# Kernel optimization log

Measured on AMD Instinct MI355X. Metric: run time of the kernel, lower is better.

The kernel has to match this reference:

```python
import jax, jax.numpy as jnp
import numpy as np

LN_EPS = 1e-5
WKV_EPS = 1e-8


def _layernorm(x, g, b):
    mu = jnp.mean(x, axis=-1, keepdims=True)
    var = jnp.mean((x - mu) ** 2, axis=-1, keepdims=True)
    return (x - mu) * jax.lax.rsqrt(var + LN_EPS) * g + b


def setup_inputs() -> dict:
    key = jax.random.key(0)
    ks = jax.random.split(key, 16)
    B, S, D, F = 4, 2048, 1024, 4096
    xavier_d = float(np.sqrt(6.0 / (D + D)))
    xavier_df = float(np.sqrt(6.0 / (D + F)))
    u = lambda k, sh, s: jax.random.uniform(k, sh, jnp.float32, -s, s)
    return {
        "x": jax.random.normal(ks[0], (B, S, D), jnp.float32),
        "ln1_g": jnp.ones((D,), jnp.float32),
        "ln1_b": jnp.zeros((D,), jnp.float32),
        "ln2_g": jnp.ones((D,), jnp.float32),
        "ln2_b": jnp.zeros((D,), jnp.float32),
        "Wr": u(ks[1], (D, D), xavier_d),
        "Ww": u(ks[2], (D, D), xavier_d),
        "Wk": u(ks[3], (D, D), xavier_d),
        "Wv": u(ks[4], (D, D), xavier_d),
        "Wo": u(ks[5], (D, D), xavier_d),
        "time_decay": jax.random.uniform(ks[6], (D,), jnp.float32, -1.0, 0.0),
        "time_first": jax.random.uniform(ks[7], (D,), jnp.float32, -1.0, 1.0),
        "Wkey": u(ks[8], (F, D), xavier_df),
        "Wval": u(ks[9], (D, F), xavier_df),
        "Wrec": u(ks[10], (D, D), xavier_d),
    }


def _time_mix(xn, Wr, Ww, Wk, Wv, Wo, time_decay):
    # xn: [B,S,D]
    r = jax.nn.sigmoid(jnp.einsum('bsd,ed->bse', xn, Wr))
    w = -jnp.exp(jnp.einsum('bsd,ed->bse', xn, Ww))
    k = jnp.einsum('bsd,ed->bse', xn, Wk)
    v = jnp.einsum('bsd,ed->bse', xn, Wv)
    ewk = jnp.exp(w + k)  # [B,S,D]
    decay = jnp.exp(time_decay)  # [D]

    def step(carry, inp):
        num, den = carry
        e, vt = inp
        num = decay * num + e * vt
        den = decay * den + e
        wkv = num / (den + WKV_EPS)
        return (num, den), wkv

    B, S, D = xn.shape
    init = (jnp.zeros((B, D), xn.dtype), jnp.zeros((B, D), xn.dtype))
    (num_f, den_f), wkv = jax.lax.scan(
        step, init, (jnp.swapaxes(ewk, 0, 1), jnp.swapaxes(v, 0, 1)))
    wkv = jnp.swapaxes(wkv, 0, 1)  # [B,S,D]
    out = jnp.einsum('bsd,ed->bse', r * wkv, Wo)
    final_state = jnp.stack([num_f, den_f], axis=1)  # [B,2,D]
    return out, final_state


def _channel_mix(xn, Wkey, Wval, Wrec):
    k = jnp.einsum('bsd,fd->bsf', xn, Wkey)
    k = jnp.square(jax.nn.relu(k))
    v = jnp.einsum('bsf,df->bsd', k, Wval)
    r = jax.nn.sigmoid(jnp.einsum('bsd,ed->bse', xn, Wrec))
    return r * v


def reference(x, ln1_g, ln1_b, ln2_g, ln2_b, Wr, Ww, Wk, Wv, Wo,
              time_decay, time_first, Wkey, Wval, Wrec):
    tm, new_state = _time_mix(_layernorm(x, ln1_g, ln1_b),
                              Wr, Ww, Wk, Wv, Wo, time_decay)
    x = x + tm
    x = x + _channel_mix(_layernorm(x, ln2_g, ln2_b), Wkey, Wval, Wrec)
    return x, new_state
```

## Files before the change

### kernel.cpp

```cpp
#include <hip/hip_runtime.h>
#include <hip/hip_bf16.h>
#include <cstdint>
#include <cstddef>

using bf16 = __hip_bfloat16;
typedef __bf16 bf16x8 __attribute__((ext_vector_type(8)));
typedef float floatx4 __attribute__((ext_vector_type(4)));

#define LN_EPS 1e-5f
#define WKV_EPS 1e-8f

static constexpr int Bdim = 4, S = 2048, D = 1024, F = 4096;
static constexpr int M = Bdim * S;
static constexpr int NCH = 64, CH = S / NCH;
static constexpr uint32_t FP32_MAGIC = 0x3F800000u;

__device__ __forceinline__ bool is_fp32(const uint32_t* flagp) {
    return *flagp == FP32_MAGIC;
}
__device__ __forceinline__ float loadf(const void* p, size_t i, bool f32) {
    return f32 ? ((const float*)p)[i] : __bfloat162float(((const bf16*)p)[i]);
}

__device__ __forceinline__ void gload_lds16(const void* g, void* l) {
    __builtin_amdgcn_global_load_lds(
        (__attribute__((address_space(1))) void*)(g),
        (__attribute__((address_space(3))) void*)(l), 16, 0, 0);
}

__device__ __forceinline__ bf16x8 sigmoid8(bf16x8 v) {
    bf16x8 o;
    #pragma unroll
    for (int e = 0; e < 8; e++) {
        const float f = (float)v[e];
        o[e] = (__bf16)(1.0f / (1.0f + __expf(-f)));
    }
    return o;
}
__device__ __forceinline__ bf16x8 relusq8(bf16x8 v) {
    bf16x8 o;
    #pragma unroll
    for (int e = 0; e < 8; e++) {
        const float f = fmaxf((float)v[e], 0.0f);
        o[e] = (__bf16)(f * f);
    }
    return o;
}

struct WcvtArgs {
    const void* src[7];
    bf16*       dst[7];
};
__global__ __launch_bounds__(256)
void wcvt(WcvtArgs a, const uint32_t* __restrict__ flagp)
{
    const bool f32 = is_fp32(flagp);
    const int64_t idx = (int64_t)blockIdx.x * 256 + threadIdx.x;
    int seg, off;
    if (idx < (int64_t)6 * 1048576) {
        seg = (int)(idx >> 20); off = (int)(idx & 1048575);
    } else {
        seg = 6; off = (int)(idx - (int64_t)6 * 1048576);
    }
    a.dst[seg][off] = __float2bfloat16(loadf(a.src[seg], off, f32));
}
__global__ __launch_bounds__(256)
void wcvt2(const void* __restrict__ src, bf16* __restrict__ dst,
           const uint32_t* __restrict__ flagp)
{
    const bool f32 = is_fp32(flagp);
    const int idx = blockIdx.x * 256 + threadIdx.x;
    dst[idx] = __float2bfloat16(loadf(src, idx, f32));
}

enum { EPI_QKVW = 1, EPI_KR = 2, EPI_ADDX = 3, EPI_FINAL = 4 };

struct QkvwOut { bf16 *r, *g, *k, *v; };

template<int EPI>
__global__ __launch_bounds__(512, 4)
void gemm_bt(const bf16* __restrict__ A, const bf16* __restrict__ Bw,
             void* __restrict__ outp, const void* __restrict__ aux1,
             void* __restrict__ aux2, QkvwOut qo, int K, int N,
             const uint32_t* __restrict__ flagp)
{
    __shared__ __align__(16) bf16 smem[16384];
    char* smb = (char*)smem;
    const int t = threadIdx.x;
    const int tn = blockIdx.x, tm = blockIdx.y;
    const int lane = t & 63, wv = t >> 6;
    const int wm = wv & 1, wn = wv >> 1;
    const int ml = lane & 15, quad = lane >> 4;

    const size_t rowB = (size_t)K * 2;
    const int r0 = t >> 3;
    const int q0 = (t & 7) ^ (r0 & 7);
    const char* gA = (const char*)(A)  + (size_t)(tm * 128) * rowB;
    const char* gB = (const char*)(Bw) + (size_t)(tn * 128) * rowB;
    const char* a0 = gA + (size_t)r0 * rowB + q0 * 16;
    const char* a1 = a0 + 64 * rowB;
    const char* b0 = gB + (size_t)r0 * rowB + q0 * 16;
    const char* b1 = b0 + 64 * rowB;
    char* lA0 = smb + t * 16;
    char* lA1 = smb + t * 16 + 8192;
    char* lB0 = smb + t * 16 + 16384;
    char* lB1 = smb + t * 16 + 24576;

    floatx4 acc[4][2] = {};
    const int m7 = ml & 7;
    const int rq0 = ((quad)     ^ m7) * 16;
    const int rq1 = ((4 + quad) ^ m7) * 16;

    for (int k0 = 0; k0 < K; k0 += 64) {
        gload_lds16(a0, lA0);
        gload_lds16(a1, lA1);
        gload_lds16(b0, lB0);
        gload_lds16(b1, lB1);
        a0 += 128; a1 += 128; b0 += 128; b1 += 128;
        __syncthreads();
        #pragma unroll
        for (int kh = 0; kh < 2; kh++) {
            const int rq = kh ? rq1 : rq0;
            bf16x8 af[4], bfr[2];
            #pragma unroll
            for (int i = 0; i < 4; i++)
                af[i]  = *(const bf16x8*)(smb + (wm * 64 + i * 16 + ml) * 128 + rq);
            #pragma unroll
            for (int j = 0; j < 2; j++)
                bfr[j] = *(const bf16x8*)(smb + 16384 + (wn * 32 + j * 16 + ml) * 128 + rq);
            #pragma unroll
            for (int i = 0; i < 4; i++)
                #pragma unroll
                for (int j = 0; j < 2; j++)
                    acc[i][j] = __builtin_amdgcn_mfma_f32_16x16x32_bf16(af[i], bfr[j], acc[i][j], 0, 0, 0);
        }
        __syncthreads();
    }

    const bool f32 = is_fp32(flagp);
    constexpr int PS = 136;
    const int lwr = wm * 16 + quad * 4;
    const int lwc = wn * 32 + ml;
    const int rr = t >> 4;
    const int rc = (t & 15) * 8;
    #pragma unroll
    for (int i = 0; i < 4; i++) {
        __syncthreads();
        #pragma unroll
        for (int j = 0; j < 2; j++)
            #pragma unroll
            for (int rg = 0; rg < 4; rg++)
                smem[(lwr + rg) * PS + lwc + j * 16] = __float2bfloat16(acc[i][j][rg]);
        __syncthreads();
        const int gr = tm * 128 + ((rr < 16) ? (i * 16 + rr) : (64 + i * 16 + rr - 16));
        bf16x8 v = *(const bf16x8*)&smem[rr * PS + rc];
        const int gcol = tn * 128 + rc;
        if constexpr (EPI == EPI_QKVW) {
            const int seg = tn >> 3;
            bf16* dst = (seg == 0) ? qo.r : (seg == 1) ? qo.g : (seg == 2) ? qo.k : qo.v;
            const size_t i2 = (size_t)gr * 1024 + (gcol & 1023);
            if (seg == 0) v = sigmoid8(v);
            *(bf16x8*)&dst[i2] = v;
        } else if constexpr (EPI == EPI_KR) {
            if (tn < 8) {
                *(bf16x8*)&((bf16*)aux2)[(size_t)gr * 1024 + gcol] = sigmoid8(v);
            } else {
                *(bf16x8*)&((bf16*)outp)[(size_t)gr * 4096 + (gcol - 1024)] = relusq8(v);
            }
        } else if constexpr (EPI == EPI_ADDX) {
            const size_t idx = (size_t)gr * N + gcol;
            bf16x8 o;
            if (f32) {
                const float4* xp = (const float4*)((const float*)aux1 + idx);
                const float4 xa = xp[0], xb = xp[1];
                o[0] = (__bf16)((float)v[0] + xa.x); o[1] = (__bf16)((float)v[1] + xa.y);
                o[2] = (__bf16)((float)v[2] + xa.z); o[3] = (__bf16)((float)v[3] + xa.w);
                o[4] = (__bf16)((float)v[4] + xb.x); o[5] = (__bf16)((float)v[5] + xb.y);
                o[6] = (__bf16)((float)v[6] + xb.z); o[7] = (__bf16)((float)v[7] + xb.w);
            } else {
                const bf16x8 xv = *(const bf16x8*)((const bf16*)aux1 + idx);
                #pragma unroll
                for (int e = 0; e < 8; e++) o[e] = (__bf16)((float)v[e] + (float)xv[e]);
            }
            *(bf16x8*)((bf16*)outp + idx) = o;
        } else {
            const size_t idx = (size_t)gr * N + gcol;
            const bf16x8 x2v = *(const bf16x8*)((const bf16*)aux1 + idx);
            const bf16x8 rv  = *(const bf16x8*)((const bf16*)aux2 + idx);
            float ov[8];
            #pragma unroll
            for (int e = 0; e < 8; e++)
                ov[e] = (float)x2v[e] + (float)rv[e] * (float)v[e];
            if (f32) {
                float4 f0 = { ov[0], ov[1], ov[2], ov[3] };
                float4 f1 = { ov[4], ov[5], ov[6], ov[7] };
                float4* op = (float4*)((float*)outp + idx);
                op[0] = f0; op[1] = f1;
            } else {
                bf16x8 o;
                #pragma unroll
                for (int e = 0; e < 8; e++) o[e] = (__bf16)ov[e];
                *(bf16x8*)((bf16*)outp + idx) = o;
            }
        }
    }
}

#define BARR  __builtin_amdgcn_s_barrier()
#define LGKM0 asm volatile("s_waitcnt lgkmcnt(0)" ::: "memory")
#define CFENCE asm volatile("" ::: "memory")

#define LDA256(d, mh) do { \
    _Pragma("unroll") for (int il = 0; il < 4; il++) \
    _Pragma("unroll") for (int kh = 0; kh < 2; kh++) \
        af[il][kh] = *(const bf16x8*)(smem + (d) * 65536 + \
            (wm * 128 + ((mh) * 4 + il) * 16 + ml) * 128 + rq[kh]); \
} while (0)

#define LDB256(d, nh) do { \
    _Pragma("unroll") for (int jl = 0; jl < 2; jl++) \
    _Pragma("unroll") for (int kh = 0; kh < 2; kh++) \
        bfr[jl][kh] = *(const bf16x8*)(smem + (d) * 65536 + 32768 + \
            (wn * 64 + ((nh) * 2 + jl) * 16 + ml) * 128 + rq[kh]); \
} while (0)

#define MMA256(mh, nh) do { \
    _Pragma("unroll") for (int il = 0; il < 4; il++) \
    _Pragma("unroll") for (int jl = 0; jl < 2; jl++) \
    _Pragma("unroll") for (int kh = 0; kh < 2; kh++) \
        acc[(mh) * 4 + il][(nh) * 2 + jl] = __builtin_amdgcn_mfma_f32_16x16x32_bf16( \
            af[il][kh], bfr[jl][kh], acc[(mh) * 4 + il][(nh) * 2 + jl], 0, 0, 0); \
} while (0)

#define STAGE_A256(d, h, kb) do { \
    gload_lds16(gA + (size_t)(h) * 128 * rowB + (kb), smem + (d) * 65536 + (h) * 16384 + t * 16); \
    gload_lds16(gA + ((size_t)(h) * 128 + 64) * rowB + (kb), smem + (d) * 65536 + (h) * 16384 + 8192 + t * 16); \
} while (0)

#define STAGE_B256(d, h, kb) do { \
    gload_lds16(gB + (size_t)(h) * 128 * rowB + (kb), smem + (d) * 65536 + 32768 + (h) * 16384 + t * 16); \
    gload_lds16(gB + ((size_t)(h) * 128 + 64) * rowB + (kb), smem + (d) * 65536 + 32768 + (h) * 16384 + 8192 + t * 16); \
} while (0)

#define PH_MID() do { BARR; LGKM0; __builtin_amdgcn_s_setprio(1); } while (0)
#define PH_END() do { __builtin_amdgcn_s_setprio(0); BARR; } while (0)

template<int EPI>
__global__ __launch_bounds__(512)
void gemm256(const bf16* __restrict__ A, const bf16* __restrict__ Bw,
             void* __restrict__ outp, const void* __restrict__ aux1,
             void* __restrict__ aux2, QkvwOut qo, int K, int N,
             const uint32_t* __restrict__ flagp)
{
    __shared__ __align__(16) char smem[131072];
    (void)N; (void)aux1; (void)flagp;
    const int t = threadIdx.x;
    const int tn = blockIdx.x, tm = blockIdx.y;
    const int lane = t & 63, wv = t >> 6;
    const int wm = wv & 1, wn = wv >> 1;
    const int ml = lane & 15, quad = lane >> 4;

    const size_t rowB = (size_t)K * 2;
    const int r0 = t >> 3;
    const int q0 = (t & 7) ^ (r0 & 7);
    const char* gA = (const char*)(A)  + (size_t)(tm * 256) * rowB + (size_t)r0 * rowB + q0 * 16;
    const char* gB = (const char*)(Bw) + (size_t)(tn * 256) * rowB + (size_t)r0 * rowB + q0 * 16;

    floatx4 acc[8][4] = {};
    bf16x8 af[4][2], bfr[2][2];
    const int m7 = ml & 7;
    const int rq[2] = { ((quad) ^ m7) * 16, ((4 + quad) ^ m7) * 16 };

    const int NT = K >> 6;
    STAGE_A256(0, 0, (size_t)0);
    STAGE_A256(0, 1, (size_t)0);
    STAGE_B256(0, 0, (size_t)0);
    STAGE_B256(0, 1, (size_t)0);
    const size_t kbp = (size_t)((NT > 1) ? 1 : 0) * 128;
    STAGE_A256(1, 0, kbp);
    STAGE_A256(1, 1, kbp);
    asm volatile("s_waitcnt vmcnt(4)" ::: "memory");
    BARR;

    for (int tt = 0; tt < NT; ++tt) {
        const int d = tt & 1;
        const size_t kb1 = (size_t)((tt + 1 < NT) ? tt + 1 : NT - 1) * 128;
        const size_t kb2 = (size_t)((tt + 2 < NT) ? tt + 2 : NT - 1) * 128;
        LDA256(d, 0); LDB256(d, 0);
        STAGE_B256(d ^ 1, 0, kb1);
        STAGE_B256(d ^ 1, 1, kb1);
        PH_MID(); MMA256(0, 0); PH_END();
        LDB256(d, 1);
        PH_MID(); MMA256(0, 1); PH_END();
        LDA256(d, 1);
        PH_MID(); MMA256(1, 1); PH_END();
        LDB256(d, 0);
        CFENCE;
        STAGE_A256(d, 0, kb2);
        STAGE_A256(d, 1, kb2);
        PH_MID(); MMA256(1, 0);
        asm volatile("s_waitcnt vmcnt(4)" ::: "memory");
        PH_END();
    }
    asm volatile("s_waitcnt vmcnt(0)" ::: "memory");
    BARR;

    bf16* sm = (bf16*)smem;
    constexpr int PS = 264;
    const int rr = t >> 4;
    const int rc = (t & 15) * 16;
    #pragma unroll
    for (int p = 0; p < 8; ++p) {
        __syncthreads();
        if (wm == (p >> 2)) {
            const int i0 = (p & 3) * 2;
            #pragma unroll
            for (int f = 0; f < 2; ++f)
                #pragma unroll
                for (int j = 0; j < 4; ++j)
                    #pragma unroll
                    for (int rg = 0; rg < 4; ++rg)
                        sm[(f * 16 + quad * 4 + rg) * PS + wn * 64 + j * 16 + ml] =
                            __float2bfloat16(acc[i0 + f][j][rg]);
        }
        __syncthreads();
        const int gr = tm * 256 + p * 32 + rr;
        bf16x8 v0 = *(const bf16x8*)&sm[rr * PS + rc];
        bf16x8 v1 = *(const bf16x8*)&sm[rr * PS + rc + 8];
        if constexpr (EPI == EPI_QKVW) {
            const int seg = tn >> 2;
            bf16* dst = (seg == 0) ? qo.r : (seg == 1) ? qo.g : (seg == 2) ? qo.k : qo.v;
            const size_t idx = (size_t)gr * 1024 + (tn & 3) * 256 + rc;
            if (seg == 0) { v0 = sigmoid8(v0); v1 = sigmoid8(v1); }
            *(bf16x8*)&dst[idx] = v0;
            *(bf16x8*)&dst[idx + 8] = v1;
        } else {
            if (tn < 4) {
                bf16* dst = (bf16*)aux2;
                const size_t idx = (size_t)gr * 1024 + tn * 256 + rc;
                *(bf16x8*)&dst[idx] = sigmoid8(v0);
                *(bf16x8*)&dst[idx + 8] = sigmoid8(v1);
            } else {
                bf16* dst = (bf16*)outp;
                const size_t idx = (size_t)gr * 4096 + (tn - 4) * 256 + rc;
                *(bf16x8*)&dst[idx] = relusq8(v0);
                *(bf16x8*)&dst[idx + 8] = relusq8(v1);
            }
        }
    }
}

#undef BARR
#undef LGKM0
#undef CFENCE
#undef LDA256
#undef LDB256
#undef MMA256
#undef STAGE_A256
#undef STAGE_B256
#undef PH_MID
#undef PH_END

template<bool IN_WS>
__global__ __launch_bounds__(256)
void ln_kernel(const void* __restrict__ x, const void* __restrict__ g,
               const void* __restrict__ b, bf16* __restrict__ out,
               const uint32_t* __restrict__ flagp)
{
    const bool f32 = is_fp32(flagp);
    const int row = blockIdx.x;
    const int t = threadIdx.x;
    const size_t base = (size_t)row * D;
    float v[4];
    #pragma unroll
    for (int i = 0; i < 4; i++) {
        const size_t c = base + t + 256 * i;
        if constexpr (IN_WS) v[i] = __bfloat162float(((const bf16*)x)[c]);
        else                 v[i] = loadf(x, c, f32);
    }
    float s = v[0] + v[1] + v[2] + v[3];
    float q = v[0]*v[0] + v[1]*v[1] + v[2]*v[2] + v[3]*v[3];
    #pragma unroll
    for (int off = 32; off > 0; off >>= 1) {
        s += __shfl_down(s, off);
        q += __shfl_down(q, off);
    }
    __shared__ float rs_[4], rq_[4];
    const int wv = t >> 6, lane = t & 63;
    if (lane == 0) { rs_[wv] = s; rq_[wv] = q; }
    __syncthreads();
    const float St = rs_[0] + rs_[1] + rs_[2] + rs_[3];
    const float Qt = rq_[0] + rq_[1] + rq_[2] + rq_[3];
    const float mean = St * (1.0f / 1024.0f);
    const float var  = Qt * (1.0f / 1024.0f) - mean * mean;
    const float rstd = rsqrtf(var + LN_EPS);
    #pragma unroll
    for (int i = 0; i < 4; i++) {
        const int c = t + 256 * i;
        const float gv = loadf(g, c, f32);
        const float bv = loadf(b, c, f32);
        out[base + c] = __float2bfloat16((v[i] - mean) * rstd * gv + bv);
    }
}

__global__ __launch_bounds__(256)
void scan_a(const bf16* __restrict__ gw, const bf16* __restrict__ kk,
            const bf16* __restrict__ vbuf, const void* __restrict__ td,
            float* __restrict__ numc, float* __restrict__ denc,
            const uint32_t* __restrict__ flagp)
{
    const bool f32 = is_fp32(flagp);
    const int idx = blockIdx.x * 256 + threadIdx.x;
    const int d = idx & (D - 1);
    const int c = (idx >> 10) & (NCH - 1);
    const int b = idx >> 16;
    const float a = __expf(loadf(td, d, f32));
    size_t p = ((size_t)b * S + (size_t)c * CH) * D + d;
    float num = 0.f, den = 0.f;
    for (int ts = 0; ts < CH; ts++) {
        const float g  = __bfloat162float(gw[p]);
        const float kv = __bfloat162float(kk[p]);
        const float e  = __expf(kv - __expf(g));
        const float vv = __bfloat162float(vbuf[p]);
        num = fmaf(a, num, e * vv);
        den = fmaf(a, den, e);
        p += D;
    }
    const size_t slot = ((size_t)b * NCH + c) * D + d;
    numc[slot] = num;
    denc[slot] = den;
}

__global__ __launch_bounds__(256)
void scan_b(float* __restrict__ numc, float* __restrict__ denc,
            const void* __restrict__ td, void* __restrict__ d_out,
            const uint32_t* __restrict__ flagp)
{
    const bool f32 = is_fp32(flagp);
    const int idx = blockIdx.x * 256 + threadIdx.x;
    const int d = idx & (D - 1);
    const int b = idx >> 10;
    const float aL = __expf(loadf(td, d, f32) * (float)CH);
    float cn = 0.f, cd = 0.f;
    for (int c = 0; c < NCH; c++) {
        const size_t slot = ((size_t)b * NCH + c) * D + d;
        const float ln = numc[slot], ld = denc[slot];
        numc[slot] = cn;
        denc[slot] = cd;
        cn = fmaf(aL, cn, ln);
        cd = fmaf(aL, cd, ld);
    }
    const size_t i0 = (size_t)b * 2 * D + d;
    const size_t i1 = i0 + D;
    const size_t off = (size_t)M * D;
    if (f32) {
        ((float*)d_out)[off + i0] = cn;
        ((float*)d_out)[off + i1] = cd;
    } else {
        ((bf16*)d_out)[off + i0] = __float2bfloat16(cn);
        ((bf16*)d_out)[off + i1] = __float2bfloat16(cd);
    }
}

__global__ __launch_bounds__(256)
void scan_c(const bf16* __restrict__ gw, const bf16* __restrict__ kk,
            const bf16* __restrict__ vbuf, bf16* __restrict__ rbuf,
            const float* __restrict__ numc, const float* __restrict__ denc,
            const void* __restrict__ td, const uint32_t* __restrict__ flagp)
{
    const bool f32 = is_fp32(flagp);
    const int idx = blockIdx.x * 256 + threadIdx.x;
    const int d = idx & (D - 1);
    const int c = (idx >> 10) & (NCH - 1);
    const int b = idx >> 16;
    const float a = __expf(loadf(td, d, f32));
    const size_t slot = ((size_t)b * NCH + c) * D + d;
    float num = numc[slot], den = denc[slot];
    size_t p = ((size_t)b * S + (size_t)c * CH) * D + d;
    for (int ts = 0; ts < CH; ts++) {
        const float g  = __bfloat162float(gw[p]);
        const float kv = __bfloat162float(kk[p]);
        const float e  = __expf(kv - __expf(g));
        const float vv = __bfloat162float(vbuf[p]);
        num = fmaf(a, num, e * vv);
        den = fmaf(a, den, e);
        const float wkv = num / (den + WKV_EPS);
        const float r = __bfloat162float(rbuf[p]);
        rbuf[p] = __float2bfloat16(r * wkv);
        p += D;
    }
}

extern "C" void kernel_launch(void* const* d_in, const int* in_sizes, int n_in,
                              void* d_out, int out_size, void* d_ws, size_t ws_size,
                              hipStream_t stream)
{
    const void* x     = d_in[0];
    const void* ln1_g = d_in[1];
    const void* ln1_b = d_in[2];
    const void* ln2_g = d_in[3];
    const void* ln2_b = d_in[4];
    const void* Wr    = d_in[5];
    const void* Ww    = d_in[6];
    const void* Wk    = d_in[7];
    const void* Wv    = d_in[8];
    const void* Wo    = d_in[9];
    const void* td    = d_in[10];
    const void* Wkey  = d_in[12];
    const void* Wval  = d_in[13];
    const void* Wrec  = d_in[14];
    const uint32_t* flagp = (const uint32_t*)ln1_g;

    #define MB(x) ((size_t)(x) << 20)
    char* ws = (char*)d_ws;
    bf16*  xnb    = (bf16*) (ws + MB(0));
    bf16*  wWval2 = (bf16*) (ws + MB(0));
    bf16*  gw     = (bf16*) (ws + MB(16));
    bf16*  kk     = (bf16*) (ws + MB(32));
    bf16*  vbuf   = (bf16*) (ws + MB(48));
    bf16*  wqkvw  = (bf16*) (ws + MB(64));
    bf16*  wWo    = (bf16*) (ws + MB(72));
    float* numc   = (float*)(ws + MB(74));
    float* denc   = (float*)(ws + MB(75));
    bf16*  kbuf   = (bf16*) (ws + MB(16));
    bf16*  rbuf   = (bf16*) (ws + MB(80));
    bf16*  x2     = (bf16*) (ws + MB(96));
    bf16*  wrk    = (bf16*) (ws + MB(112));
    #undef MB

    dim3 blk(256);
    dim3 blkG(512);
    dim3 gQ(4096 / 256, M / 256);
    dim3 gKR(5120 / 256, M / 256);
    dim3 gN1(D / 128, M / 128);

    WcvtArgs wa;
    wa.src[0] = Wr;   wa.dst[0] = wqkvw;
    wa.src[1] = Ww;   wa.dst[1] = wqkvw + (size_t)1 * 1048576;
    wa.src[2] = Wk;   wa.dst[2] = wqkvw + (size_t)2 * 1048576;
    wa.src[3] = Wv;   wa.dst[3] = wqkvw + (size_t)3 * 1048576;
    wa.src[4] = Wo;   wa.dst[4] = wWo;
    wa.src[5] = Wrec; wa.dst[5] = wrk;
    wa.src[6] = Wkey; wa.dst[6] = wrk + (size_t)1048576;

    QkvwOut qo = { rbuf, gw, kk, vbuf };
    QkvwOut q0 = { nullptr, nullptr, nullptr, nullptr };

    wcvt<<<(10 * 1048576) / 256, blk, 0, stream>>>(wa, flagp);
    ln_kernel<false><<<M, blk, 0, stream>>>(x, ln1_g, ln1_b, xnb, flagp);
    gemm256<EPI_QKVW><<<gQ, blkG, 0, stream>>>(xnb, wqkvw, nullptr, nullptr, nullptr, qo, D, 4096, flagp);
    scan_a<<<(Bdim * NCH * D) / 256, blk, 0, stream>>>(gw, kk, vbuf, td, numc, denc, flagp);
    scan_b<<<(Bdim * D) / 256,       blk, 0, stream>>>(numc, denc, td, d_out, flagp);
    scan_c<<<(Bdim * NCH * D) / 256, blk, 0, stream>>>(gw, kk, vbuf, rbuf, numc, denc, td, flagp);
    gemm_bt<EPI_ADDX><<<gN1, blkG, 0, stream>>>(rbuf, wWo, x2, x, nullptr, q0, D, D, flagp);
    ln_kernel<true><<<M, blk, 0, stream>>>(x2, ln2_g, ln2_b, xnb, flagp);
    gemm256<EPI_KR><<<gKR, blkG, 0, stream>>>(xnb, wrk, kbuf, nullptr, rbuf, q0, D, 5120, flagp);
    wcvt2<<<(4 * 1048576) / 256, blk, 0, stream>>>(Wval, wWval2, flagp);
    gemm_bt<EPI_FINAL><<<gN1, blkG, 0, stream>>>(kbuf, wWval2, d_out, x2, rbuf, q0, F, D, flagp);
}
```

Baseline: 529.5 us.

## Restructure GEMM main loop into k-half stages with register double buffering

Reorganizes the 256x256 GEMM LDS layout so each 64-wide k tile is split into two 32-wide k halves stored in separate buffers. The loop now ping-pongs A fragments between two register sets and overlaps LDS reads with MFMA phases, issuing global-to-LDS loads at finer granularity with vmcnt(6) waits. It also adds a launch_bounds occupancy hint of 2. The aim is to hide LDS and global latency better, at the cost of more registers and more complex barrier ordering that could introduce hazards.

```diff
diff --git a/kernel.cpp b/kernel.cpp
--- a/kernel.cpp
+++ b/kernel.cpp
@@ -207,46 +207,44 @@
 }
 
 #define BARR  __builtin_amdgcn_s_barrier()
-#define LGKM0 asm volatile("s_waitcnt lgkmcnt(0)" ::: "memory")
-#define CFENCE asm volatile("" ::: "memory")
-
-#define LDA256(d, mh) do { \
+#define PRIO1 __builtin_amdgcn_s_setprio(1)
+#define PRIO0 __builtin_amdgcn_s_setprio(0)
+#define VM6   asm volatile("s_waitcnt vmcnt(6)" ::: "memory")
+
+#define AOFF(dd, khh) (((dd) * 2 + (khh)) * 16384)
+#define BOFF(dd, khh) (65536 + ((dd) * 2 + (khh)) * 16384)
+
+#define DSA(DST, dd, khh, mhh) do { \
     _Pragma("unroll") for (int il = 0; il < 4; il++) \
-    _Pragma("unroll") for (int kh = 0; kh < 2; kh++) \
-        af[il][kh] = *(const bf16x8*)(smem + (d) * 65536 + \
-            (wm * 128 + ((mh) * 4 + il) * 16 + ml) * 128 + rq[kh]); \
+        DST[il] = *(const bf16x8*)(smem + AOFF(dd, khh) + \
+            (wm * 64 + (mhh) * 32 + il * 8 + mlh) * 128 + p16); \
 } while (0)
 
-#define LDB256(d, nh) do { \
-    _Pragma("unroll") for (int jl = 0; jl < 2; jl++) \
-    _Pragma("unroll") for (int kh = 0; kh < 2; kh++) \
-        bfr[jl][kh] = *(const bf16x8*)(smem + (d) * 65536 + 32768 + \
-            (wn * 64 + ((nh) * 2 + jl) * 16 + ml) * 128 + rq[kh]); \
+#define DSB(DST, dd, khh) do { \
+    _Pragma("unroll") for (int j = 0; j < 4; j++) \
+        DST[j] = *(const bf16x8*)(smem + BOFF(dd, khh) + \
+            (wn * 32 + j * 8 + mlh) * 128 + p16); \
 } while (0)
 
-#define MMA256(mh, nh) do { \
+#define MMA(mhh, AF, BF) do { \
     _Pragma("unroll") for (int il = 0; il < 4; il++) \
-    _Pragma("unroll") for (int jl = 0; jl < 2; jl++) \
-    _Pragma("unroll") for (int kh = 0; kh < 2; kh++) \
-        acc[(mh) * 4 + il][(nh) * 2 + jl] = __builtin_amdgcn_mfma_f32_16x16x32_bf16( \
-            af[il][kh], bfr[jl][kh], acc[(mh) * 4 + il][(nh) * 2 + jl], 0, 0, 0); \
+    _Pragma("unroll") for (int j = 0; j < 4; j++) \
+        acc[(mhh) * 4 + il][j] = __builtin_amdgcn_mfma_f32_16x16x32_bf16( \
+            AF[il], BF[j], acc[(mhh) * 4 + il][j], 0, 0, 0); \
 } while (0)
 
-#define STAGE_A256(d, h, kb) do { \
-    gload_lds16(gA + (size_t)(h) * 128 * rowB + (kb), smem + (d) * 65536 + (h) * 16384 + t * 16); \
-    gload_lds16(gA + ((size_t)(h) * 128 + 64) * rowB + (kb), smem + (d) * 65536 + (h) * 16384 + 8192 + t * 16); \
+#define STGA(dd, khh, gsrc) do { \
+    gload_lds16((gsrc) + off0,           smem + AOFF(dd, khh) + t * 16); \
+    gload_lds16((gsrc) + off0 + offHalf, smem + AOFF(dd, khh) + 8192 + t * 16); \
 } while (0)
 
-#define STAGE_B256(d, h, kb) do { \
-    gload_lds16(gB + (size_t)(h) * 128 * rowB + (kb), smem + (d) * 65536 + 32768 + (h) * 16384 + t * 16); \
-    gload_lds16(gB + ((size_t)(h) * 128 + 64) * rowB + (kb), smem + (d) * 65536 + 32768 + (h) * 16384 + 8192 + t * 16); \
+#define STGB(dd, khh, gsrc) do { \
+    gload_lds16((gsrc) + off0,           smem + BOFF(dd, khh) + t * 16); \
+    gload_lds16((gsrc) + off0 + offHalf, smem + BOFF(dd, khh) + 8192 + t * 16); \
 } while (0)
 
-#define PH_MID() do { BARR; LGKM0; __builtin_amdgcn_s_setprio(1); } while (0)
-#define PH_END() do { __builtin_amdgcn_s_setprio(0); BARR; } while (0)
-
 template<int EPI>
-__global__ __launch_bounds__(512)
+__global__ __launch_bounds__(512, 2)
 void gemm256(const bf16* __restrict__ A, const bf16* __restrict__ Bw,
              void* __restrict__ outp, const void* __restrict__ aux1,
              void* __restrict__ aux2, QkvwOut qo, int K, int N,
@@ -259,52 +257,58 @@
     const int lane = t & 63, wv = t >> 6;
     const int wm = wv & 1, wn = wv >> 1;
     const int ml = lane & 15, quad = lane >> 4;
+    const int mlh = ml >> 1;
+    const int p16 = (((ml & 1) * 4 + quad) ^ (mlh & 7)) * 16;
 
     const size_t rowB = (size_t)K * 2;
-    const int r0 = t >> 3;
-    const int q0 = (t & 7) ^ (r0 & 7);
-    const char* gA = (const char*)(A)  + (size_t)(tm * 256) * rowB + (size_t)r0 * rowB + q0 * 16;
-    const char* gB = (const char*)(Bw) + (size_t)(tn * 256) * rowB + (size_t)r0 * rowB + q0 * 16;
+    const int l0 = t >> 3;
+    const int q0p = (t & 7) ^ (l0 & 7);
+    const size_t off0 = (size_t)(2 * l0 + (q0p >> 2)) * rowB + (q0p & 3) * 16;
+    const size_t offHalf = (size_t)128 * rowB;
+    const char* gA = (const char*)(A)  + (size_t)(tm * 256) * rowB;
+    const char* gB = (const char*)(Bw) + (size_t)(tn * 256) * rowB;
 
     floatx4 acc[8][4] = {};
-    bf16x8 af[4][2], bfr[2][2];
-    const int m7 = ml & 7;
-    const int rq[2] = { ((quad) ^ m7) * 16, ((4 + quad) ^ m7) * 16 };
+    bf16x8 af_e[4], af_o[4], bfr0[4], bfr1[4];
 
     const int NT = K >> 6;
-    STAGE_A256(0, 0, (size_t)0);
-    STAGE_A256(0, 1, (size_t)0);
-    STAGE_B256(0, 0, (size_t)0);
-    STAGE_B256(0, 1, (size_t)0);
-    const size_t kbp = (size_t)((NT > 1) ? 1 : 0) * 128;
-    STAGE_A256(1, 0, kbp);
-    STAGE_A256(1, 1, kbp);
-    asm volatile("s_waitcnt vmcnt(4)" ::: "memory");
+    STGA(0, 0, gA);
+    STGB(0, 0, gB);
+    STGA(0, 1, gA + 64);
+    STGB(0, 1, gB + 64);
+    const size_t c1 = (size_t)((NT > 1) ? 1 : 0) * 128;
+    STGA(1, 0, gA + c1);
+    STGB(1, 0, gB + c1);
+    asm volatile("s_waitcnt vmcnt(8)" ::: "memory");
     BARR;
-
-    for (int tt = 0; tt < NT; ++tt) {
-        const int d = tt & 1;
-        const size_t kb1 = (size_t)((tt + 1 < NT) ? tt + 1 : NT - 1) * 128;
-        const size_t kb2 = (size_t)((tt + 2 < NT) ? tt + 2 : NT - 1) * 128;
-        LDA256(d, 0); LDB256(d, 0);
-        STAGE_B256(d ^ 1, 0, kb1);
-        STAGE_B256(d ^ 1, 1, kb1);
-        PH_MID(); MMA256(0, 0); PH_END();
-        LDB256(d, 1);
-        PH_MID(); MMA256(0, 1); PH_END();
-        LDA256(d, 1);
-        PH_MID(); MMA256(1, 1); PH_END();
-        LDB256(d, 0);
-        CFENCE;
-        STAGE_A256(d, 0, kb2);
-        STAGE_A256(d, 1, kb2);
-        PH_MID(); MMA256(1, 0);
-        asm volatile("s_waitcnt vmcnt(4)" ::: "memory");
-        PH_END();
+    DSA(af_e, 0, 0, 0);
+    DSB(bfr0, 0, 0);
+
+    for (int T = 0; T < NT; ++T) {
+        const int d = T & 1, e = d ^ 1;
+        const size_t s1 = (size_t)((T + 1 < NT) ? T + 1 : NT - 1) * 128;
+        const size_t s2 = (size_t)((T + 2 < NT) ? T + 2 : NT - 1) * 128;
+        DSA(af_o, d, 0, 1);
+        STGA(e, 1, gA + s1 + 64);
+        BARR; PRIO1; MMA(0, af_e, bfr0); PRIO0; BARR;
+        VM6;
+        DSA(af_e, d, 1, 0);
+        DSB(bfr1, d, 1);
+        STGB(e, 1, gB + s1 + 64);
+        BARR; PRIO1; MMA(1, af_o, bfr0); PRIO0; BARR;
+        DSA(af_o, d, 1, 1);
+        STGA(d, 0, gA + s2);
+        BARR; PRIO1; MMA(0, af_e, bfr1); PRIO0; BARR;
+        VM6;
+        DSA(af_e, e, 0, 0);
+        DSB(bfr0, e, 0);
+        STGB(d, 0, gB + s2);
+        BARR; PRIO1; MMA(1, af_o, bfr1); PRIO0; BARR;
     }
     asm volatile("s_waitcnt vmcnt(0)" ::: "memory");
     BARR;
 
+    const bool f32x = is_fp32(flagp); (void)f32x;
     bf16* sm = (bf16*)smem;
     constexpr int PS = 264;
     const int rr = t >> 4;
@@ -351,15 +355,16 @@
 }
 
 #undef BARR
-#undef LGKM0
-#undef CFENCE
-#undef LDA256
-#undef LDB256
-#undef MMA256
-#undef STAGE_A256
-#undef STAGE_B256
-#undef PH_MID
-#undef PH_END
+#undef PRIO1
+#undef PRIO0
+#undef VM6
+#undef AOFF
+#undef BOFF
+#undef DSA
+#undef DSB
+#undef MMA
+#undef STGA
+#undef STGB
 
 template<bool IN_WS>
 __global__ __launch_bounds__(256)
```

Result: no change. 533.2 us (+0.7%).
